# Optimization experiments

Hardware: AMD Instinct MI355X
Metric: run time of the kernel (lower is better)

Reference implementation:

```python
import jax, jax.numpy as jnp
import numpy as np

B, P, DE, DD, DA = 256, 196, 2048, 512, 512

def setup_inputs() -> dict:
    key = jax.random.key(0)
    ks = jax.random.split(key, 8)
    s_enc = 1.0 / np.sqrt(DE)
    s_dec = 1.0 / np.sqrt(DD)
    s_att = 1.0 / np.sqrt(DA)
    return {
        "encoder_out": jax.random.normal(ks[0], (B, P, DE), dtype=jnp.float32),
        "decoder_hidden": jax.random.normal(ks[1], (B, DD), dtype=jnp.float32),
        "W_enc": jax.random.uniform(ks[2], (DE, DA), jnp.float32, -s_enc, s_enc),
        "b_enc": jax.random.uniform(ks[3], (DA,), jnp.float32, -s_enc, s_enc),
        "W_dec": jax.random.uniform(ks[4], (DD, DA), jnp.float32, -s_dec, s_dec),
        "b_dec": jax.random.uniform(ks[5], (DA,), jnp.float32, -s_dec, s_dec),
        "W_full": jax.random.uniform(ks[6], (DA, 1), jnp.float32, -s_att, s_att),
        "b_full": jax.random.uniform(ks[7], (1,), jnp.float32, -s_att, s_att),
    }

def reference(encoder_out, decoder_hidden, W_enc, b_enc, W_dec, b_dec, W_full, b_full):
    # att1: [B,P,DA]; att2: [B,DA]
    att1 = jnp.einsum('bpe,ea->bpa', encoder_out, W_enc) + b_enc
    att2 = decoder_hidden @ W_dec + b_dec
    # broadcast add + relu + project to scalar score per position
    att = jnp.einsum('bpa,a->bp', jax.nn.relu(att1 + att2[:, None, :]), W_full[:, 0]) + b_full[0]
    alpha = jax.nn.softmax(att, axis=1)  # [B,P]
    context_vector = jnp.einsum('bpe,bp->be', encoder_out, alpha)  # [B,DE]
    return (context_vector, alpha)
```

## Files before the change

### kernel.cpp

```cpp
#include <hip/hip_runtime.h>
#include <hip/hip_bf16.h>
#include <cstddef>

#define B_   256
#define P_   196
#define DE_  2048
#define DD_  512
#define DA_  512
#define M_   (B_*P_)

#define BM   64
#define KT   32

typedef __attribute__((ext_vector_type(4))) float f32x4;
typedef __attribute__((ext_vector_type(8))) short s16x8;

static __device__ __forceinline__ short f2bf(float x) {
    __hip_bfloat16 h = __float2bfloat16(x);
    return *reinterpret_cast<short*>(&h);
}

#define GLOAD_LDS16(g, l) __builtin_amdgcn_global_load_lds( \
    (const __attribute__((address_space(1))) void*)(g),     \
    (__attribute__((address_space(3))) void*)(l), 16, 0, 0)

__global__ void pack_wenc(const float* __restrict__ W, __hip_bfloat16* __restrict__ out) {
    __shared__ float lds[KT][128 + 1];
    const int kt = blockIdx.x;
    const int n0 = blockIdx.y * 128;
    const int t  = threadIdx.x;
#pragma unroll
    for (int i = 0; i < 16; ++i) {
        int e  = t + i * 256;
        int kl = e >> 7;
        int nl = e & 127;
        lds[kl][nl] = W[(size_t)(kt * KT + kl) * DA_ + n0 + nl];
    }
    __syncthreads();
    short* o16 = reinterpret_cast<short*>(out);
#pragma unroll
    for (int i = 0; i < 2; ++i) {
        int task = t + i * 256;
        int nl   = task >> 2;
        int s    = task & 3;
        int n    = n0 + nl;
        int sp   = s ^ ((n >> 1) & 3);
        s16x8 w;
#pragma unroll
        for (int j = 0; j < 8; ++j)
            w[j] = f2bf(lds[s * 8 + j][nl]);
        *reinterpret_cast<s16x8*>(o16 + (size_t)kt * (DA_ * KT) + n * KT + sp * 8) = w;
    }
}

__global__ __launch_bounds__(512) void att2_kernel(
        const float* __restrict__ dh, const float* __restrict__ W_dec,
        const float* __restrict__ b_dec, const float* __restrict__ b_enc,
        float* __restrict__ att2p) {
    __shared__ float s_dh[DD_];
    const int b = blockIdx.x;
    const int a = threadIdx.x;
    s_dh[a] = dh[(size_t)b * DD_ + a];
    __syncthreads();
    float acc = 0.f;
#pragma unroll 8
    for (int k = 0; k < DD_; ++k)
        acc += s_dh[k] * W_dec[(size_t)k * DA_ + a];
    att2p[(size_t)b * DA_ + a] = acc + b_dec[a] + b_enc[a];
}

__global__ __launch_bounds__(256, 2) void gemm_att(
        const float* __restrict__ enc, const __hip_bfloat16* __restrict__ Bp,
        const float* __restrict__ att2p, const float* __restrict__ Wfull,
        const float* __restrict__ bfull, float* __restrict__ att) {
    __shared__ __hip_bfloat16 a_lds0[BM * KT];
    __shared__ __hip_bfloat16 a_lds1[BM * KT];
    __shared__ __hip_bfloat16 b_lds0[DA_ * KT];
    __shared__ __hip_bfloat16 b_lds1[DA_ * KT];
    __shared__ float red[BM][4];

    const int tid  = threadIdx.x;
    const int wave = tid >> 6;
    const int lane = tid & 63;
    const int g    = lane >> 4;
    const int c    = lane & 15;
    const int block_row = blockIdx.x * BM;
    const int nbase = wave * 128;
    const int slot8 = (g ^ ((c >> 1) & 3)) * 8;

    const int ar = tid >> 2;
    const int aq = tid & 3;
    const int a_woff = ar * KT + (aq ^ ((ar >> 1) & 3)) * 8;
    const float* ap = enc + (size_t)(block_row + ar) * DE_ + aq * 8;

    f32x4 acc[4][8] = {};
    f32x4 pa0, pa1, pb0, pb1;

#define STORE_A(dstbase, v0, v1) do {                                   \
        s16x8 w_;                                                       \
        w_[0]=f2bf((v0).x); w_[1]=f2bf((v0).y); w_[2]=f2bf((v0).z); w_[3]=f2bf((v0).w); \
        w_[4]=f2bf((v1).x); w_[5]=f2bf((v1).y); w_[6]=f2bf((v1).z); w_[7]=f2bf((v1).w); \
        *reinterpret_cast<s16x8*>((dstbase) + a_woff) = w_;             \
    } while (0)

#define ISSUE_B(T, dstb) do {                                           \
        const char* bs_ = (const char*)Bp + (size_t)(T) * (DA_*KT*2) + (size_t)tid * 16; \
        char* bd_ = (char*)(dstb) + (size_t)tid * 16;                   \
        _Pragma("unroll")                                               \
        for (int i_ = 0; i_ < 8; ++i_)                                  \
            GLOAD_LDS16(bs_ + i_ * 4096, bd_ + i_ * 4096);              \
    } while (0)

#define FRAGS_MFMA(abuf, bbuf) do {                                     \
        s16x8 af[4], bf[8];                                             \
        _Pragma("unroll")                                               \
        for (int mt = 0; mt < 4; ++mt)                                  \
            af[mt] = *reinterpret_cast<const s16x8*>((abuf) + (mt*16 + c) * KT + slot8); \
        _Pragma("unroll")                                               \
        for (int nt = 0; nt < 8; ++nt)                                  \
            bf[nt] = *reinterpret_cast<const s16x8*>((bbuf) + (nbase + nt*16 + c) * KT + slot8); \
        _Pragma("unroll")                                               \
        for (int mt = 0; mt < 4; ++mt)                                  \
            _Pragma("unroll")                                           \
            for (int nt = 0; nt < 8; ++nt)                              \
                acc[mt][nt] = __builtin_amdgcn_mfma_f32_16x16x32_bf16(  \
                                  af[mt], bf[nt], acc[mt][nt], 0, 0, 0);\
    } while (0)

#define FENCE_AFTER_BARRIER() do {                                      \
        asm volatile("" ::: "memory");                                  \
        __builtin_amdgcn_sched_barrier(0);                              \
    } while (0)

    pa0 = *reinterpret_cast<const f32x4*>(ap);
    pa1 = *reinterpret_cast<const f32x4*>(ap + 4);
    ISSUE_B(0, b_lds0);
    pb0 = *reinterpret_cast<const f32x4*>(ap + KT);
    pb1 = *reinterpret_cast<const f32x4*>(ap + KT + 4);
    STORE_A(a_lds0, pa0, pa1);
    asm volatile("s_waitcnt vmcnt(2) lgkmcnt(0)" ::: "memory");
    __builtin_amdgcn_s_barrier();
    FENCE_AFTER_BARRIER();

    const float* ap_it = ap;
#pragma clang loop unroll(disable)
    for (int kt = 0; kt < 62; kt += 2) {
        ISSUE_B(kt + 1, b_lds1);
        pa0 = *reinterpret_cast<const f32x4*>(ap_it + 2 * KT);
        pa1 = *reinterpret_cast<const f32x4*>(ap_it + 2 * KT + 4);
        FRAGS_MFMA(a_lds0, b_lds0);
        STORE_A(a_lds1, pb0, pb1);
        asm volatile("s_waitcnt vmcnt(2) lgkmcnt(0)" ::: "memory");
        __builtin_amdgcn_s_barrier();
        FENCE_AFTER_BARRIER();
        ISSUE_B(kt + 2, b_lds0);
        pb0 = *reinterpret_cast<const f32x4*>(ap_it + 3 * KT);
        pb1 = *reinterpret_cast<const f32x4*>(ap_it + 3 * KT + 4);
        FRAGS_MFMA(a_lds1, b_lds1);
        STORE_A(a_lds0, pa0, pa1);
        asm volatile("s_waitcnt vmcnt(2) lgkmcnt(0)" ::: "memory");
        __builtin_amdgcn_s_barrier();
        FENCE_AFTER_BARRIER();
        ap_it += 2 * KT;
    }
    ISSUE_B(63, b_lds1);
    FRAGS_MFMA(a_lds0, b_lds0);
    STORE_A(a_lds1, pb0, pb1);
    asm volatile("s_waitcnt vmcnt(0) lgkmcnt(0)" ::: "memory");
    __builtin_amdgcn_s_barrier();
    FENCE_AFTER_BARRIER();
    FRAGS_MFMA(a_lds1, b_lds1);

    const int b0    = block_row / P_;
    const int b1    = min(b0 + 1, B_ - 1);
    const int split = (b0 + 1) * P_;
    float wf[8], a20[8], a21[8];
#pragma unroll
    for (int nt = 0; nt < 8; ++nt) {
        const int n = nbase + nt * 16 + c;
        wf[nt]  = Wfull[n];
        a20[nt] = att2p[(size_t)b0 * DA_ + n];
        a21[nt] = att2p[(size_t)b1 * DA_ + n];
    }
#pragma unroll
    for (int mt = 0; mt < 4; ++mt) {
#pragma unroll
        for (int q = 0; q < 4; ++q) {
            const int row_local = mt * 16 + g * 4 + q;
            const int R = block_row + row_local;
            const bool hi = (R >= split);
            float s = 0.f;
#pragma unroll
            for (int nt = 0; nt < 8; ++nt) {
                float a2 = hi ? a21[nt] : a20[nt];
                float v  = acc[mt][nt][q] + a2;
                v = fmaxf(v, 0.f);
                s += v * wf[nt];
            }
#pragma unroll
            for (int off = 1; off < 16; off <<= 1)
                s += __shfl_xor(s, off, 64);
            if (c == 0) red[row_local][wave] = s;
        }
    }
    __syncthreads();
    if (tid < BM) {
        float t = 0.f;
#pragma unroll
        for (int w = 0; w < 4; ++w) t += red[tid][w];
        att[block_row + tid] = t + bfull[0];
    }
#undef STORE_A
#undef ISSUE_B
#undef FRAGS_MFMA
#undef FENCE_AFTER_BARRIER
}

__global__ __launch_bounds__(256) void softmax_kernel(
        const float* __restrict__ att, float* __restrict__ alpha) {
    const int b = blockIdx.x;
    const int t = threadIdx.x;
    __shared__ float sred[4];
    float v = (t < P_) ? att[(size_t)b * P_ + t] : -1e30f;
    float m = v;
#pragma unroll
    for (int off = 1; off < 64; off <<= 1) m = fmaxf(m, __shfl_xor(m, off, 64));
    if ((t & 63) == 0) sred[t >> 6] = m;
    __syncthreads();
    const float mall = fmaxf(fmaxf(sred[0], sred[1]), fmaxf(sred[2], sred[3]));
    __syncthreads();
    float e = (t < P_) ? expf(v - mall) : 0.f;
    float s = e;
#pragma unroll
    for (int off = 1; off < 64; off <<= 1) s += __shfl_xor(s, off, 64);
    if ((t & 63) == 0) sred[t >> 6] = s;
    __syncthreads();
    const float stot = sred[0] + sred[1] + sred[2] + sred[3];
    if (t < P_) alpha[(size_t)b * P_ + t] = e / stot;
}

__global__ __launch_bounds__(256) void context_kernel(
        const float* __restrict__ enc, const float* __restrict__ alpha,
        float* __restrict__ ctx) {
    const int b = blockIdx.x;
    const int e = blockIdx.y * 1024 + threadIdx.x * 4;
    __shared__ float s_alpha[P_];
    if (threadIdx.x < P_) s_alpha[threadIdx.x] = alpha[(size_t)b * P_ + threadIdx.x];
    __syncthreads();
    f32x4 acc = {0.f, 0.f, 0.f, 0.f};
    const float* base = enc + (size_t)b * P_ * DE_ + e;
#pragma unroll 4
    for (int p = 0; p < P_; ++p) {
        f32x4 v = *reinterpret_cast<const f32x4*>(base + (size_t)p * DE_);
        acc += s_alpha[p] * v;
    }
    *reinterpret_cast<f32x4*>(ctx + (size_t)b * DE_ + e) = acc;
}

extern "C" void kernel_launch(void* const* d_in, const int* in_sizes, int n_in,
                              void* d_out, int out_size, void* d_ws, size_t ws_size,
                              hipStream_t stream) {
    const float* enc    = (const float*)d_in[0];
    const float* dh     = (const float*)d_in[1];
    const float* W_enc  = (const float*)d_in[2];
    const float* b_enc  = (const float*)d_in[3];
    const float* W_dec  = (const float*)d_in[4];
    const float* b_dec  = (const float*)d_in[5];
    const float* W_full = (const float*)d_in[6];
    const float* b_full = (const float*)d_in[7];

    float* out       = (float*)d_out;
    float* ctx_out   = out;
    float* alpha_out = out + (size_t)B_ * DE_;

    char* ws = (char*)d_ws;
    __hip_bfloat16* Bp = (__hip_bfloat16*)ws;
    float* att2p = (float*)(ws + 2u * 1024 * 1024);
    float* att   = (float*)(ws + 2u * 1024 * 1024 + 512u * 1024);

    pack_wenc   <<<dim3(64, 4),     256, 0, stream>>>(W_enc, Bp);
    att2_kernel <<<B_,              512, 0, stream>>>(dh, W_dec, b_dec, b_enc, att2p);
    gemm_att    <<<M_ / BM,         256, 0, stream>>>(enc, Bp, att2p, W_full, b_full, att);
    softmax_kernel<<<B_,            256, 0, stream>>>(att, alpha_out);
    context_kernel<<<dim3(B_, 2),   256, 0, stream>>>(enc, alpha_out, ctx_out);
}
```

Before: 282.7 us.

## Load B fragments directly from global into registers, dropping B LDS staging

The W_enc packing kernel now writes bf16 weights in the exact per-lane MFMA fragment order, so each wave reads its B fragments straight from global memory into registers instead of staging the 512x32 B tile through double-buffered LDS. This frees 64 KB of LDS per block, which could allow more blocks per CU, and removes LDS reads and the vmcnt waits tied to the LDS DMA. In exchange, B loads now hit L2/global once per wave with less latency hiding, because the fragments are only issued one tile ahead in registers. The A pipeline is also reorganised to prefetch two tiles ahead, and the pack kernel now uses one block per K tile.

```diff
diff --git a/kernel.cpp b/kernel.cpp
--- a/kernel.cpp
+++ b/kernel.cpp
@@ -11,6 +11,7 @@
 
 #define BM   64
 #define KT   32
+#define NKT  (DE_/KT)
 
 typedef __attribute__((ext_vector_type(4))) float f32x4;
 typedef __attribute__((ext_vector_type(8))) short s16x8;
@@ -20,36 +21,30 @@
     return *reinterpret_cast<short*>(&h);
 }
 
-#define GLOAD_LDS16(g, l) __builtin_amdgcn_global_load_lds( \
-    (const __attribute__((address_space(1))) void*)(g),     \
-    (__attribute__((address_space(3))) void*)(l), 16, 0, 0)
-
-__global__ void pack_wenc(const float* __restrict__ W, __hip_bfloat16* __restrict__ out) {
-    __shared__ float lds[KT][128 + 1];
+__global__ __launch_bounds__(256) void pack_wenc(
+        const float* __restrict__ W, __hip_bfloat16* __restrict__ out) {
+    __shared__ float lds[KT][DA_];
     const int kt = blockIdx.x;
-    const int n0 = blockIdx.y * 128;
     const int t  = threadIdx.x;
 #pragma unroll
-    for (int i = 0; i < 16; ++i) {
-        int e  = t + i * 256;
-        int kl = e >> 7;
-        int nl = e & 127;
-        lds[kl][nl] = W[(size_t)(kt * KT + kl) * DA_ + n0 + nl];
-    }
-    __syncthreads();
-    short* o16 = reinterpret_cast<short*>(out);
-#pragma unroll
-    for (int i = 0; i < 2; ++i) {
-        int task = t + i * 256;
-        int nl   = task >> 2;
-        int s    = task & 3;
-        int n    = n0 + nl;
-        int sp   = s ^ ((n >> 1) & 3);
+    for (int i = 0; i < 64; ++i) {
+        int e = i * 256 + t;
+        int k = e >> 9, n = e & 511;
+        lds[k][n] = W[(size_t)(kt * KT + k) * DA_ + n];
+    }
+    __syncthreads();
+    short* o = reinterpret_cast<short*>(out) + (size_t)kt * (32 * 64 * 8);
+#pragma unroll
+    for (int i = 0; i < 8; ++i) {
+        int idx  = i * 256 + t;
+        int gf   = idx >> 6;
+        int lane = idx & 63;
+        int g = lane >> 4, c = lane & 15;
         s16x8 w;
 #pragma unroll
         for (int j = 0; j < 8; ++j)
-            w[j] = f2bf(lds[s * 8 + j][nl]);
-        *reinterpret_cast<s16x8*>(o16 + (size_t)kt * (DA_ * KT) + n * KT + sp * 8) = w;
+            w[j] = f2bf(lds[g * 8 + j][gf * 16 + c]);
+        *reinterpret_cast<s16x8*>(o + (size_t)idx * 8) = w;
     }
 }
 
@@ -75,8 +70,6 @@
         const float* __restrict__ bfull, float* __restrict__ att) {
     __shared__ __hip_bfloat16 a_lds0[BM * KT];
     __shared__ __hip_bfloat16 a_lds1[BM * KT];
-    __shared__ __hip_bfloat16 b_lds0[DA_ * KT];
-    __shared__ __hip_bfloat16 b_lds1[DA_ * KT];
     __shared__ float red[BM][4];
 
     const int tid  = threadIdx.x;
@@ -93,83 +86,75 @@
     const int a_woff = ar * KT + (aq ^ ((ar >> 1) & 3)) * 8;
     const float* ap = enc + (size_t)(block_row + ar) * DE_ + aq * 8;
 
+    const s16x8* bp = reinterpret_cast<const s16x8*>(Bp) + (size_t)(wave * 8) * 64 + lane;
+
     f32x4 acc[4][8] = {};
-    f32x4 pa0, pa1, pb0, pb1;
-
-#define STORE_A(dstbase, v0, v1) do {                                   \
+    f32x4 pX0, pX1, pY0, pY1;
+    s16x8 bf[8];
+
+#define ISSUE_A(v0, v1, T) do {                                         \
+        const int tt_ = (T) > 63 ? 63 : (T);                            \
+        v0 = *reinterpret_cast<const f32x4*>(ap + tt_ * KT);            \
+        v1 = *reinterpret_cast<const f32x4*>(ap + tt_ * KT + 4);        \
+    } while (0)
+
+#define ISSUE_BF(T) do {                                                \
+        _Pragma("unroll")                                               \
+        for (int nt_ = 0; nt_ < 8; ++nt_)                               \
+            bf[nt_] = bp[((size_t)(T) * 32 + nt_) * 64];                \
+    } while (0)
+
+#define STORE_A(dst, v0, v1) do {                                       \
         s16x8 w_;                                                       \
         w_[0]=f2bf((v0).x); w_[1]=f2bf((v0).y); w_[2]=f2bf((v0).z); w_[3]=f2bf((v0).w); \
         w_[4]=f2bf((v1).x); w_[5]=f2bf((v1).y); w_[6]=f2bf((v1).z); w_[7]=f2bf((v1).w); \
-        *reinterpret_cast<s16x8*>((dstbase) + a_woff) = w_;             \
-    } while (0)
-
-#define ISSUE_B(T, dstb) do {                                           \
-        const char* bs_ = (const char*)Bp + (size_t)(T) * (DA_*KT*2) + (size_t)tid * 16; \
-        char* bd_ = (char*)(dstb) + (size_t)tid * 16;                   \
+        *reinterpret_cast<s16x8*>((dst) + a_woff) = w_;                 \
+    } while (0)
+
+#define AFRAGS_MFMA(abuf) do {                                          \
+        s16x8 af[4];                                                    \
         _Pragma("unroll")                                               \
-        for (int i_ = 0; i_ < 8; ++i_)                                  \
-            GLOAD_LDS16(bs_ + i_ * 4096, bd_ + i_ * 4096);              \
-    } while (0)
-
-#define FRAGS_MFMA(abuf, bbuf) do {                                     \
-        s16x8 af[4], bf[8];                                             \
+        for (int mt_ = 0; mt_ < 4; ++mt_)                               \
+            af[mt_] = *reinterpret_cast<const s16x8*>((abuf) + (mt_*16 + c) * KT + slot8); \
         _Pragma("unroll")                                               \
-        for (int mt = 0; mt < 4; ++mt)                                  \
-            af[mt] = *reinterpret_cast<const s16x8*>((abuf) + (mt*16 + c) * KT + slot8); \
-        _Pragma("unroll")                                               \
-        for (int nt = 0; nt < 8; ++nt)                                  \
-            bf[nt] = *reinterpret_cast<const s16x8*>((bbuf) + (nbase + nt*16 + c) * KT + slot8); \
-        _Pragma("unroll")                                               \
-        for (int mt = 0; mt < 4; ++mt)                                  \
+        for (int nt_ = 0; nt_ < 8; ++nt_)                               \
             _Pragma("unroll")                                           \
-            for (int nt = 0; nt < 8; ++nt)                              \
-                acc[mt][nt] = __builtin_amdgcn_mfma_f32_16x16x32_bf16(  \
-                                  af[mt], bf[nt], acc[mt][nt], 0, 0, 0);\
-    } while (0)
-
-#define FENCE_AFTER_BARRIER() do {                                      \
-        asm volatile("" ::: "memory");                                  \
+            for (int mt_ = 0; mt_ < 4; ++mt_)                           \
+                acc[mt_][nt_] = __builtin_amdgcn_mfma_f32_16x16x32_bf16(\
+                                    af[mt_], bf[nt_], acc[mt_][nt_], 0, 0, 0); \
+    } while (0)
+
+#define BAR() do {                                                      \
+        asm volatile("s_waitcnt lgkmcnt(0)" ::: "memory");              \
+        __builtin_amdgcn_s_barrier();                                   \
         __builtin_amdgcn_sched_barrier(0);                              \
     } while (0)
 
-    pa0 = *reinterpret_cast<const f32x4*>(ap);
-    pa1 = *reinterpret_cast<const f32x4*>(ap + 4);
-    ISSUE_B(0, b_lds0);
-    pb0 = *reinterpret_cast<const f32x4*>(ap + KT);
-    pb1 = *reinterpret_cast<const f32x4*>(ap + KT + 4);
-    STORE_A(a_lds0, pa0, pa1);
-    asm volatile("s_waitcnt vmcnt(2) lgkmcnt(0)" ::: "memory");
-    __builtin_amdgcn_s_barrier();
-    FENCE_AFTER_BARRIER();
-
-    const float* ap_it = ap;
+    ISSUE_A(pX0, pX1, 0);
+    ISSUE_A(pY0, pY1, 1);
+    ISSUE_BF(0);
+    STORE_A(a_lds0, pX0, pX1);
+    ISSUE_A(pX0, pX1, 2);
+    BAR();
+
 #pragma clang loop unroll(disable)
-    for (int kt = 0; kt < 62; kt += 2) {
-        ISSUE_B(kt + 1, b_lds1);
-        pa0 = *reinterpret_cast<const f32x4*>(ap_it + 2 * KT);
-        pa1 = *reinterpret_cast<const f32x4*>(ap_it + 2 * KT + 4);
-        FRAGS_MFMA(a_lds0, b_lds0);
-        STORE_A(a_lds1, pb0, pb1);
-        asm volatile("s_waitcnt vmcnt(2) lgkmcnt(0)" ::: "memory");
-        __builtin_amdgcn_s_barrier();
-        FENCE_AFTER_BARRIER();
-        ISSUE_B(kt + 2, b_lds0);
-        pb0 = *reinterpret_cast<const f32x4*>(ap_it + 3 * KT);
-        pb1 = *reinterpret_cast<const f32x4*>(ap_it + 3 * KT + 4);
-        FRAGS_MFMA(a_lds1, b_lds1);
-        STORE_A(a_lds0, pa0, pa1);
-        asm volatile("s_waitcnt vmcnt(2) lgkmcnt(0)" ::: "memory");
-        __builtin_amdgcn_s_barrier();
-        FENCE_AFTER_BARRIER();
-        ap_it += 2 * KT;
-    }
-    ISSUE_B(63, b_lds1);
-    FRAGS_MFMA(a_lds0, b_lds0);
-    STORE_A(a_lds1, pb0, pb1);
-    asm volatile("s_waitcnt vmcnt(0) lgkmcnt(0)" ::: "memory");
-    __builtin_amdgcn_s_barrier();
-    FENCE_AFTER_BARRIER();
-    FRAGS_MFMA(a_lds1, b_lds1);
+    for (int t = 0; t < 62; t += 2) {
+        STORE_A(a_lds1, pY0, pY1);
+        ISSUE_A(pY0, pY1, t + 3);
+        AFRAGS_MFMA(a_lds0);
+        ISSUE_BF(t + 1);
+        BAR();
+        STORE_A(a_lds0, pX0, pX1);
+        ISSUE_A(pX0, pX1, t + 4);
+        AFRAGS_MFMA(a_lds1);
+        ISSUE_BF(t + 2);
+        BAR();
+    }
+    STORE_A(a_lds1, pY0, pY1);
+    AFRAGS_MFMA(a_lds0);
+    ISSUE_BF(63);
+    BAR();
+    AFRAGS_MFMA(a_lds1);
 
     const int b0    = block_row / P_;
     const int b1    = min(b0 + 1, B_ - 1);
@@ -210,10 +195,11 @@
         for (int w = 0; w < 4; ++w) t += red[tid][w];
         att[block_row + tid] = t + bfull[0];
     }
+#undef ISSUE_A
+#undef ISSUE_BF
 #undef STORE_A
-#undef ISSUE_B
-#undef FRAGS_MFMA
-#undef FENCE_AFTER_BARRIER
+#undef AFRAGS_MFMA
+#undef BAR
 }
 
 __global__ __launch_bounds__(256) void softmax_kernel(
@@ -278,7 +264,7 @@
     float* att2p = (float*)(ws + 2u * 1024 * 1024);
     float* att   = (float*)(ws + 2u * 1024 * 1024 + 512u * 1024);
 
-    pack_wenc   <<<dim3(64, 4),     256, 0, stream>>>(W_enc, Bp);
+    pack_wenc   <<<NKT,             256, 0, stream>>>(W_enc, Bp);
     att2_kernel <<<B_,              512, 0, stream>>>(dh, W_dec, b_dec, b_enc, att2p);
     gemm_att    <<<M_ / BM,         256, 0, stream>>>(enc, Bp, att2p, W_full, b_full, att);
     softmax_kernel<<<B_,            256, 0, stream>>>(att, alpha_out);
```

Result: faster. 275.3 us (-2.6%).
